# Kernel optimization log

Measured on AMD Instinct MI355X. Metric: run time of the kernel, lower is better.

The kernel has to match this reference:

```python
import jax, jax.numpy as jnp
import numpy as np

N_NODES = 50000
N_EDGES = 800000
IN_CH = 128
OUT_CH = 64
HEADS = 1
NEG_SLOPE = 0.2

def _glorot(key, shape):
    stdv = np.sqrt(6.0 / (shape[-2] + shape[-1]))
    return jax.random.uniform(key, shape, jnp.float32, -stdv, stdv)

def setup_inputs() -> dict:
    key = jax.random.key(0)
    k1, k2, k3, k4, k5 = jax.random.split(key, 5)
    x = jax.random.normal(k1, (N_NODES, IN_CH), jnp.float32)
    src = jax.random.randint(k2, (N_EDGES,), 0, N_NODES)
    dst = jax.random.randint(k3, (N_EDGES,), 0, N_NODES)
    # ensure no pre-existing self loops (remove_self_loops is then identity)
    dst = jnp.where(src == dst, (dst + 1) % N_NODES, dst)
    edge_index = jnp.stack([src, dst]).astype(jnp.int64)
    weight = _glorot(k4, (IN_CH, HEADS * OUT_CH))
    att = _glorot(k5, (1, HEADS, 2 * OUT_CH))
    bias = jnp.zeros((OUT_CH,), jnp.float32)
    return {"x": x, "edge_index": edge_index, "weight": weight, "att": att, "bias": bias}

def reference(x, edge_index, weight, att, bias):
    N = x.shape[0]
    # linear projection -> [N, heads, out]
    h = (x @ weight).reshape(N, HEADS, OUT_CH)
    # add self loops (input guaranteed free of self loops)
    loops = jnp.arange(N, dtype=edge_index.dtype)
    src = jnp.concatenate([edge_index[0], loops])  # source j
    dst = jnp.concatenate([edge_index[1], loops])  # target i
    x_j = h[src]   # [E+N, heads, out]
    x_i = h[dst]
    # attention logits: (cat([x_i, x_j]) * att).sum(-1) -> [E+N, heads]
    alpha = jnp.concatenate([x_i, x_j], axis=-1)
    alpha = (alpha * att).sum(axis=-1)
    alpha = jax.nn.leaky_relu(alpha, NEG_SLOPE)
    # segment softmax over destination nodes
    amax = jax.ops.segment_max(alpha, dst, num_segments=N)
    e = jnp.exp(alpha - amax[dst])
    esum = jax.ops.segment_sum(e, dst, num_segments=N)
    alpha = e / (esum[dst] + 1e-16)
    # message + scatter-add aggregation
    msg = x_j * alpha[:, :, None]
    out = jax.ops.segment_sum(msg, dst, num_segments=N)  # [N, heads, out]
    out = out.mean(axis=1) + bias
    # F.normalize (L2, dim=1, eps=1e-12); dropout is eval-mode identity
    norm = jnp.maximum(jnp.linalg.norm(out, axis=1, keepdims=True), 1e-12)
    return out / norm
```

## Files before the change

kernel.cpp:

```cpp
#include <hip/hip_runtime.h>
#include <math.h>

#define IN_CH 128
#define OUT_CH 64
#define NEG_SLOPE 0.2f
#define CAP 64

__device__ __forceinline__ unsigned short f2bf(float f) {
    unsigned u = __float_as_uint(f);
    unsigned r = (u + 0x7FFFu + ((u >> 16) & 1u)) >> 16;
    return (unsigned short)r;
}

__device__ __forceinline__ bool sniff_is64(const void* edges) {
    const unsigned* up = (const unsigned*)edges;
    bool is64 = true;
#pragma unroll
    for (int k = 0; k < 16; k++) is64 = is64 && (up[2 * k + 1] == 0u);
    return is64;
}

__global__ __launch_bounds__(256) void k_mm_cs(
        const float* __restrict__ x, const float* __restrict__ W,
        const float* __restrict__ att, unsigned short* __restrict__ h16,
        float* __restrict__ asrc, float* __restrict__ adst, int N,
        const void* __restrict__ edges, int* __restrict__ counts,
        int* __restrict__ slots, int* __restrict__ oflow_cnt,
        int2* __restrict__ oflow, int E, int mmb, int csb) {
    __shared__ float Ws[IN_CH * OUT_CH];
    int t = threadIdx.x;
    int bid = blockIdx.x;
    int lo = min(mmb, csb), M2 = 2 * lo;
    int role, id;
    if (bid < M2) { role = bid & 1; id = bid >> 1; }
    else          { role = (mmb > csb) ? 0 : 1; id = bid - M2 + lo; }

    if (role == 1) {
        int e0 = (id * 256 + t) * 4;
        if (e0 >= E) return;
        int s[4], d[4];
        bool full = (e0 + 3 < E);
        if (full) {
            if (sniff_is64(edges)) {
                const long long* p = (const long long*)edges;
#pragma unroll
                for (int i = 0; i < 4; i++) {
                    s[i] = (int)__builtin_nontemporal_load(p + e0 + i);
                    d[i] = (int)__builtin_nontemporal_load(p + (size_t)E + e0 + i);
                }
            } else {
                const int* p = (const int*)edges;
#pragma unroll
                for (int i = 0; i < 4; i++) {
                    s[i] = __builtin_nontemporal_load(p + e0 + i);
                    d[i] = __builtin_nontemporal_load(p + E + e0 + i);
                }
            }
#pragma unroll
            for (int i = 0; i < 4; i++) {
                int r = atomicAdd(counts + d[i], 1);
                if (r < CAP) {
                    slots[((size_t)d[i] << 6) + r] = s[i];
                } else {
                    int p2 = atomicAdd(oflow_cnt, 1);
                    oflow[p2] = make_int2(s[i], d[i]);
                }
            }
        } else {
            bool is64 = sniff_is64(edges);
            for (int i = 0; i < 4; i++) {
                if (e0 + i >= E) break;
                int sv, dv;
                if (is64) {
                    const long long* p = (const long long*)edges;
                    sv = (int)p[e0 + i];
                    dv = (int)p[(size_t)E + e0 + i];
                } else {
                    const int* p = (const int*)edges;
                    sv = p[e0 + i];
                    dv = p[E + e0 + i];
                }
                int r = atomicAdd(counts + dv, 1);
                if (r < CAP) {
                    slots[((size_t)dv << 6) + r] = sv;
                } else {
                    int p2 = atomicAdd(oflow_cnt, 1);
                    oflow[p2] = make_int2(sv, dv);
                }
            }
        }
        return;
    }

    for (int i = t * 4; i < IN_CH * OUT_CH; i += 256 * 4)
        *(float4*)&Ws[i] = *(const float4*)&W[i];
    int cg = t & 15, g = t >> 4;
    float4 att_d = *(const float4*)&att[cg * 4];
    float4 att_s = *(const float4*)&att[64 + cg * 4];
    __syncthreads();

    int n0 = id * 64 + g * 4;
    int nn[4];
#pragma unroll
    for (int m = 0; m < 4; m++) nn[m] = min(n0 + m, N - 1);

    float4 acc[4];
#pragma unroll
    for (int m = 0; m < 4; m++) acc[m] = make_float4(0.f, 0.f, 0.f, 0.f);

#pragma unroll 2
    for (int k4 = 0; k4 < IN_CH / 4; k4++) {
        float4 xv[4];
#pragma unroll
        for (int m = 0; m < 4; m++)
            xv[m] = *(const float4*)&x[(size_t)nn[m] * IN_CH + k4 * 4];
        float4 wv[4];
#pragma unroll
        for (int j = 0; j < 4; j++)
            wv[j] = *(const float4*)&Ws[(k4 * 4 + j) * OUT_CH + cg * 4];
#pragma unroll
        for (int m = 0; m < 4; m++) {
            acc[m].x = fmaf(xv[m].x, wv[0].x, acc[m].x);
            acc[m].y = fmaf(xv[m].x, wv[0].y, acc[m].y);
            acc[m].z = fmaf(xv[m].x, wv[0].z, acc[m].z);
            acc[m].w = fmaf(xv[m].x, wv[0].w, acc[m].w);
            acc[m].x = fmaf(xv[m].y, wv[1].x, acc[m].x);
            acc[m].y = fmaf(xv[m].y, wv[1].y, acc[m].y);
            acc[m].z = fmaf(xv[m].y, wv[1].z, acc[m].z);
            acc[m].w = fmaf(xv[m].y, wv[1].w, acc[m].w);
            acc[m].x = fmaf(xv[m].z, wv[2].x, acc[m].x);
            acc[m].y = fmaf(xv[m].z, wv[2].y, acc[m].y);
            acc[m].z = fmaf(xv[m].z, wv[2].z, acc[m].z);
            acc[m].w = fmaf(xv[m].z, wv[2].w, acc[m].w);
            acc[m].x = fmaf(xv[m].w, wv[3].x, acc[m].x);
            acc[m].y = fmaf(xv[m].w, wv[3].y, acc[m].y);
            acc[m].z = fmaf(xv[m].w, wv[3].z, acc[m].z);
            acc[m].w = fmaf(xv[m].w, wv[3].w, acc[m].w);
        }
    }

#pragma unroll
    for (int m = 0; m < 4; m++) {
        int node = n0 + m;
        if (node < N) {
            ushort4 hv;
            hv.x = f2bf(acc[m].x);
            hv.y = f2bf(acc[m].y);
            hv.z = f2bf(acc[m].z);
            hv.w = f2bf(acc[m].w);
            *(ushort4*)&h16[(size_t)node * OUT_CH + cg * 4] = hv;
        }
        float pd = acc[m].x * att_d.x + acc[m].y * att_d.y +
                   acc[m].z * att_d.z + acc[m].w * att_d.w;
        float ps = acc[m].x * att_s.x + acc[m].y * att_s.y +
                   acc[m].z * att_s.z + acc[m].w * att_s.w;
#pragma unroll
        for (int msk = 1; msk < 16; msk <<= 1) {
            pd += __shfl_xor(pd, msk, 64);
            ps += __shfl_xor(ps, msk, 64);
        }
        if (cg == 0 && node < N) { adst[node] = pd; asrc[node] = ps; }
    }
}

__global__ __launch_bounds__(256) void k_agg(const unsigned short* __restrict__ h16,
                                             const int* __restrict__ slots,
                                             const int* __restrict__ counts,
                                             const int* __restrict__ oflow_cnt,
                                             const int2* __restrict__ oflow,
                                             const float* __restrict__ asrc,
                                             const float* __restrict__ adst,
                                             const float* __restrict__ bias,
                                             float* __restrict__ out, int N) {
    __shared__ float2 stage[4][64];
    int lane = threadIdx.x & 63;
    int wid = threadIdx.x >> 6;
    int node = blockIdx.x * 4 + wid;
    if (node >= N) return;
    int half = lane >> 5;
    int ch2 = (lane & 31) * 2;

    float aD = adst[node];
    float a = aD + asrc[node];
    a = a > 0.f ? a : NEG_SLOPE * a;
    float w_self = __expf(a);
    unsigned hv = *(const unsigned*)&h16[(size_t)node * OUT_CH + ch2];
    float wse = half ? 0.f : w_self;
    float accx = wse * __uint_as_float(hv << 16);
    float accy = wse * __uint_as_float(hv & 0xFFFF0000u);

    int c = counts[node];
    int cs = min(c, CAP);
    int sv = 0;
    float wv = 0.f;
    if (lane < cs) {
        sv = slots[((size_t)node << 6) + lane];
        float av = aD + asrc[sv];
        av = av > 0.f ? av : NEG_SLOPE * av;
        wv = __expf(av);
    }
    float esum_lane = wv;
    stage[wid][lane] = make_float2(__int_as_float(sv), wv);

    for (int j = 0; j < cs; j += 16) {
#pragma unroll
        for (int k = 0; k < 8; k++) {
            float2 p = stage[wid][j + 2 * k + half];
            int s = __float_as_int(p.x);
            unsigned v = *(const unsigned*)&h16[((size_t)s << 6) + ch2];
            accx = fmaf(p.y, __uint_as_float(v << 16), accx);
            accy = fmaf(p.y, __uint_as_float(v & 0xFFFF0000u), accy);
        }
    }
    accx += __shfl_xor(accx, 32, 64);
    accy += __shfl_xor(accy, 32, 64);
#pragma unroll
    for (int m = 32; m >= 1; m >>= 1) esum_lane += __shfl_xor(esum_lane, m, 64);
    float esum = esum_lane + w_self;

    int oc = *oflow_cnt;
    if (oc > 0) {
        for (int i = 0; i < oc; i++) {
            int2 e = oflow[i];
            if (e.y == node) {
                float av = aD + asrc[e.x];
                av = av > 0.f ? av : NEG_SLOPE * av;
                float w = __expf(av);
                esum += w;
                unsigned v = *(const unsigned*)&h16[((size_t)e.x << 6) + ch2];
                accx = fmaf(w, __uint_as_float(v << 16), accx);
                accy = fmaf(w, __uint_as_float(v & 0xFFFF0000u), accy);
            }
        }
    }

    float inv = 1.f / (esum + 1e-16f);
    float2 bv = *(const float2*)&bias[ch2];
    float vx = accx * inv + bv.x;
    float vy = accy * inv + bv.y;
    float ss = vx * vx + vy * vy;
#pragma unroll
    for (int m = 16; m >= 1; m >>= 1) ss += __shfl_xor(ss, m, 64);
    float rinv = 1.f / fmaxf(sqrtf(ss), 1e-12f);
    if (!half)
        *(float2*)&out[(size_t)node * OUT_CH + ch2] = make_float2(vx * rinv, vy * rinv);
}

extern "C" void kernel_launch(void* const* d_in, const int* in_sizes, int n_in,
                              void* d_out, int out_size, void* d_ws, size_t ws_size,
                              hipStream_t stream) {
    const float* x    = (const float*)d_in[0];
    const void*  edges = d_in[1];
    const float* W    = (const float*)d_in[2];
    const float* att  = (const float*)d_in[3];
    const float* bias = (const float*)d_in[4];
    float* out = (float*)d_out;

    const int N = in_sizes[0] / IN_CH;
    const int E = in_sizes[1] / 2;
    const int MMB = (N + 63) / 64;
    const int CSB = (E + 1023) / 1024;

    char* ws = (char*)d_ws;
    size_t off = 0;
    auto alloc = [&](size_t bytes) -> void* {
        void* p = ws + off;
        off += bytes;
        off = (off + 255) & ~(size_t)255;
        return p;
    };
    int*            counts   = (int*)alloc((size_t)(N + 64) * 4);
    int*            slots    = (int*)alloc((size_t)N * CAP * 4);
    int2*           oflow    = (int2*)alloc((size_t)E * 8);
    unsigned short* h16      = (unsigned short*)alloc((size_t)N * OUT_CH * 2);
    float*          asrc     = (float*)alloc((size_t)N * 4);
    float*          adst     = (float*)alloc((size_t)N * 4);
    int*            oflow_cnt = counts + N;

    hipMemsetAsync(counts, 0, (size_t)(N + 64) * 4, stream);
    k_mm_cs<<<MMB + CSB, 256, 0, stream>>>(x, W, att, h16, asrc, adst, N,
                                           edges, counts, slots, oflow_cnt,
                                           oflow, E, MMB, CSB);
    k_agg<<<(N + 3) / 4, 256, 0, stream>>>(h16, slots, counts, oflow_cnt, oflow,
                                           asrc, adst, bias, out, N);
}
```

Measured before the change: 144.5 us.

## Fuse edge bucketing and projection per block, overlapping atomics with matmul

```diff
diff --git a/kernel.cpp b/kernel.cpp
--- a/kernel.cpp
+++ b/kernel.cpp
@@ -5,6 +5,10 @@
 #define OUT_CH 64
 #define NEG_SLOPE 0.2f
 #define CAP 64
+#define EPT 4
+
+typedef long long ll2 __attribute__((ext_vector_type(2)));
+typedef int i4v __attribute__((ext_vector_type(4)));
 
 __device__ __forceinline__ unsigned short f2bf(float f) {
     unsigned u = __float_as_uint(f);
@@ -26,140 +30,134 @@
         float* __restrict__ asrc, float* __restrict__ adst, int N,
         const void* __restrict__ edges, int* __restrict__ counts,
         int* __restrict__ slots, int* __restrict__ oflow_cnt,
-        int2* __restrict__ oflow, int E, int mmb, int csb) {
-    __shared__ float Ws[IN_CH * OUT_CH];
+        int2* __restrict__ oflow, int E) {
     int t = threadIdx.x;
     int bid = blockIdx.x;
-    int lo = min(mmb, csb), M2 = 2 * lo;
-    int role, id;
-    if (bid < M2) { role = bid & 1; id = bid >> 1; }
-    else          { role = (mmb > csb) ? 0 : 1; id = bid - M2 + lo; }
-
-    if (role == 1) {
-        int e0 = (id * 256 + t) * 4;
-        if (e0 >= E) return;
-        int s[4], d[4];
-        bool full = (e0 + 3 < E);
-        if (full) {
-            if (sniff_is64(edges)) {
+
+    int e0 = (bid * 256 + t) * EPT;
+    int s[EPT], d[EPT], r[EPT];
+    bool fullcs = (e0 + EPT <= E);
+    if (fullcs) {
+        if (sniff_is64(edges)) {
+            const ll2* ps = (const ll2*)((const long long*)edges + e0);
+            const ll2* pd = (const ll2*)((const long long*)edges + (size_t)E + e0);
+            ll2 v0 = __builtin_nontemporal_load(ps);
+            ll2 v1 = __builtin_nontemporal_load(ps + 1);
+            ll2 w0 = __builtin_nontemporal_load(pd);
+            ll2 w1 = __builtin_nontemporal_load(pd + 1);
+            s[0] = (int)v0.x; s[1] = (int)v0.y; s[2] = (int)v1.x; s[3] = (int)v1.y;
+            d[0] = (int)w0.x; d[1] = (int)w0.y; d[2] = (int)w1.x; d[3] = (int)w1.y;
+        } else {
+            i4v v = __builtin_nontemporal_load((const i4v*)((const int*)edges + e0));
+            i4v w = __builtin_nontemporal_load((const i4v*)((const int*)edges + E + e0));
+            s[0] = v.x; s[1] = v.y; s[2] = v.z; s[3] = v.w;
+            d[0] = w.x; d[1] = w.y; d[2] = w.z; d[3] = w.w;
+        }
+#pragma unroll
+        for (int i = 0; i < EPT; i++) r[i] = atomicAdd(counts + d[i], 1);
+    } else if (e0 < E) {
+        bool is64 = sniff_is64(edges);
+        for (int i = 0; i < EPT && e0 + i < E; i++) {
+            int sv, dv;
+            if (is64) {
                 const long long* p = (const long long*)edges;
-#pragma unroll
-                for (int i = 0; i < 4; i++) {
-                    s[i] = (int)__builtin_nontemporal_load(p + e0 + i);
-                    d[i] = (int)__builtin_nontemporal_load(p + (size_t)E + e0 + i);
-                }
+                sv = (int)p[e0 + i];
+                dv = (int)p[(size_t)E + e0 + i];
             } else {
                 const int* p = (const int*)edges;
-#pragma unroll
-                for (int i = 0; i < 4; i++) {
-                    s[i] = __builtin_nontemporal_load(p + e0 + i);
-                    d[i] = __builtin_nontemporal_load(p + E + e0 + i);
-                }
-            }
-#pragma unroll
-            for (int i = 0; i < 4; i++) {
-                int r = atomicAdd(counts + d[i], 1);
-                if (r < CAP) {
-                    slots[((size_t)d[i] << 6) + r] = s[i];
-                } else {
-                    int p2 = atomicAdd(oflow_cnt, 1);
-                    oflow[p2] = make_int2(s[i], d[i]);
-                }
-            }
-        } else {
-            bool is64 = sniff_is64(edges);
-            for (int i = 0; i < 4; i++) {
-                if (e0 + i >= E) break;
-                int sv, dv;
-                if (is64) {
-                    const long long* p = (const long long*)edges;
-                    sv = (int)p[e0 + i];
-                    dv = (int)p[(size_t)E + e0 + i];
-                } else {
-                    const int* p = (const int*)edges;
-                    sv = p[e0 + i];
-                    dv = p[E + e0 + i];
-                }
-                int r = atomicAdd(counts + dv, 1);
-                if (r < CAP) {
-                    slots[((size_t)dv << 6) + r] = sv;
-                } else {
-                    int p2 = atomicAdd(oflow_cnt, 1);
-                    oflow[p2] = make_int2(sv, dv);
-                }
-            }
-        }
-        return;
-    }
-
-    for (int i = t * 4; i < IN_CH * OUT_CH; i += 256 * 4)
-        *(float4*)&Ws[i] = *(const float4*)&W[i];
-    int cg = t & 15, g = t >> 4;
-    float4 att_d = *(const float4*)&att[cg * 4];
-    float4 att_s = *(const float4*)&att[64 + cg * 4];
-    __syncthreads();
-
-    int n0 = id * 64 + g * 4;
-    int nn[4];
-#pragma unroll
-    for (int m = 0; m < 4; m++) nn[m] = min(n0 + m, N - 1);
-
-    float4 acc[4];
-#pragma unroll
-    for (int m = 0; m < 4; m++) acc[m] = make_float4(0.f, 0.f, 0.f, 0.f);
+                sv = p[e0 + i];
+                dv = p[E + e0 + i];
+            }
+            int rr = atomicAdd(counts + dv, 1);
+            if (rr < CAP) {
+                slots[((size_t)dv << 6) + rr] = sv;
+            } else {
+                int p2 = atomicAdd(oflow_cnt, 1);
+                oflow[p2] = make_int2(sv, dv);
+            }
+        }
+    }
+    asm volatile("" ::: "memory");
+
+    if (bid * 64 < N) {
+        int cg = t & 15, g = t >> 4;
+        float4 att_d = *(const float4*)&att[cg * 4];
+        float4 att_s = *(const float4*)&att[64 + cg * 4];
+
+        int n0 = bid * 64 + g * 4;
+        int nn[4];
+#pragma unroll
+        for (int m = 0; m < 4; m++) nn[m] = min(n0 + m, N - 1);
+
+        float4 acc[4];
+#pragma unroll
+        for (int m = 0; m < 4; m++) acc[m] = make_float4(0.f, 0.f, 0.f, 0.f);
 
 #pragma unroll 2
-    for (int k4 = 0; k4 < IN_CH / 4; k4++) {
-        float4 xv[4];
-#pragma unroll
-        for (int m = 0; m < 4; m++)
-            xv[m] = *(const float4*)&x[(size_t)nn[m] * IN_CH + k4 * 4];
-        float4 wv[4];
-#pragma unroll
-        for (int j = 0; j < 4; j++)
-            wv[j] = *(const float4*)&Ws[(k4 * 4 + j) * OUT_CH + cg * 4];
+        for (int k4 = 0; k4 < IN_CH / 4; k4++) {
+            float4 xv[4];
+#pragma unroll
+            for (int m = 0; m < 4; m++)
+                xv[m] = *(const float4*)&x[(size_t)nn[m] * IN_CH + k4 * 4];
+            float4 wv[4];
+#pragma unroll
+            for (int j = 0; j < 4; j++)
+                wv[j] = *(const float4*)&W[(k4 * 4 + j) * OUT_CH + cg * 4];
+#pragma unroll
+            for (int m = 0; m < 4; m++) {
+                acc[m].x = fmaf(xv[m].x, wv[0].x, acc[m].x);
+                acc[m].y = fmaf(xv[m].x, wv[0].y, acc[m].y);
+                acc[m].z = fmaf(xv[m].x, wv[0].z, acc[m].z);
+                acc[m].w = fmaf(xv[m].x, wv[0].w, acc[m].w);
+                acc[m].x = fmaf(xv[m].y, wv[1].x, acc[m].x);
+                acc[m].y = fmaf(xv[m].y, wv[1].y, acc[m].y);
+                acc[m].z = fmaf(xv[m].y, wv[1].z, acc[m].z);
+                acc[m].w = fmaf(xv[m].y, wv[1].w, acc[m].w);
+                acc[m].x = fmaf(xv[m].z, wv[2].x, acc[m].x);
+                acc[m].y = fmaf(xv[m].z, wv[2].y, acc[m].y);
+                acc[m].z = fmaf(xv[m].z, wv[2].z, acc[m].z);
+                acc[m].w = fmaf(xv[m].z, wv[2].w, acc[m].w);
+                acc[m].x = fmaf(xv[m].w, wv[3].x, acc[m].x);
+                acc[m].y = fmaf(xv[m].w, wv[3].y, acc[m].y);
+                acc[m].z = fmaf(xv[m].w, wv[3].z, acc[m].z);
+                acc[m].w = fmaf(xv[m].w, wv[3].w, acc[m].w);
+            }
+        }
+
 #pragma unroll
         for (int m = 0; m < 4; m++) {
-            acc[m].x = fmaf(xv[m].x, wv[0].x, acc[m].x);
-            acc[m].y = fmaf(xv[m].x, wv[0].y, acc[m].y);
-            acc[m].z = fmaf(xv[m].x, wv[0].z, acc[m].z);
-            acc[m].w = fmaf(xv[m].x, wv[0].w, acc[m].w);
-            acc[m].x = fmaf(xv[m].y, wv[1].x, acc[m].x);
-            acc[m].y = fmaf(xv[m].y, wv[1].y, acc[m].y);
-            acc[m].z = fmaf(xv[m].y, wv[1].z, acc[m].z);
-            acc[m].w = fmaf(xv[m].y, wv[1].w, acc[m].w);
-            acc[m].x = fmaf(xv[m].z, wv[2].x, acc[m].x);
-            acc[m].y = fmaf(xv[m].z, wv[2].y, acc[m].y);
-            acc[m].z = fmaf(xv[m].z, wv[2].z, acc[m].z);
-            acc[m].w = fmaf(xv[m].z, wv[2].w, acc[m].w);
-            acc[m].x = fmaf(xv[m].w, wv[3].x, acc[m].x);
-            acc[m].y = fmaf(xv[m].w, wv[3].y, acc[m].y);
-            acc[m].z = fmaf(xv[m].w, wv[3].z, acc[m].z);
-            acc[m].w = fmaf(xv[m].w, wv[3].w, acc[m].w);
-        }
-    }
-
-#pragma unroll
-    for (int m = 0; m < 4; m++) {
-        int node = n0 + m;
-        if (node < N) {
-            ushort4 hv;
-            hv.x = f2bf(acc[m].x);
-            hv.y = f2bf(acc[m].y);
-            hv.z = f2bf(acc[m].z);
-            hv.w = f2bf(acc[m].w);
-            *(ushort4*)&h16[(size_t)node * OUT_CH + cg * 4] = hv;
-        }
-        float pd = acc[m].x * att_d.x + acc[m].y * att_d.y +
-                   acc[m].z * att_d.z + acc[m].w * att_d.w;
-        float ps = acc[m].x * att_s.x + acc[m].y * att_s.y +
-                   acc[m].z * att_s.z + acc[m].w * att_s.w;
-#pragma unroll
-        for (int msk = 1; msk < 16; msk <<= 1) {
-            pd += __shfl_xor(pd, msk, 64);
-            ps += __shfl_xor(ps, msk, 64);
-        }
-        if (cg == 0 && node < N) { adst[node] = pd; asrc[node] = ps; }
+            int node = n0 + m;
+            if (node < N) {
+                ushort4 hv;
+                hv.x = f2bf(acc[m].x);
+                hv.y = f2bf(acc[m].y);
+                hv.z = f2bf(acc[m].z);
+                hv.w = f2bf(acc[m].w);
+                *(ushort4*)&h16[(size_t)node * OUT_CH + cg * 4] = hv;
+            }
+            float pd = acc[m].x * att_d.x + acc[m].y * att_d.y +
+                       acc[m].z * att_d.z + acc[m].w * att_d.w;
+            float ps = acc[m].x * att_s.x + acc[m].y * att_s.y +
+                       acc[m].z * att_s.z + acc[m].w * att_s.w;
+#pragma unroll
+            for (int msk = 1; msk < 16; msk <<= 1) {
+                pd += __shfl_xor(pd, msk, 64);
+                ps += __shfl_xor(ps, msk, 64);
+            }
+            if (cg == 0 && node < N) { adst[node] = pd; asrc[node] = ps; }
+        }
+    }
+
+    if (fullcs) {
+#pragma unroll
+        for (int i = 0; i < EPT; i++) {
+            if (r[i] < CAP) {
+                slots[((size_t)d[i] << 6) + r[i]] = s[i];
+            } else {
+                int p2 = atomicAdd(oflow_cnt, 1);
+                oflow[p2] = make_int2(s[i], d[i]);
+            }
+        }
     }
 }
 
@@ -259,7 +257,8 @@
     const int N = in_sizes[0] / IN_CH;
     const int E = in_sizes[1] / 2;
     const int MMB = (N + 63) / 64;
-    const int CSB = (E + 1023) / 1024;
+    const int CSB = (E + 256 * EPT - 1) / (256 * EPT);
+    const int NB = MMB > CSB ? MMB : CSB;
 
     char* ws = (char*)d_ws;
     size_t off = 0;
@@ -278,9 +277,8 @@
     int*            oflow_cnt = counts + N;
 
     hipMemsetAsync(counts, 0, (size_t)(N + 64) * 4, stream);
-    k_mm_cs<<<MMB + CSB, 256, 0, stream>>>(x, W, att, h16, asrc, adst, N,
-                                           edges, counts, slots, oflow_cnt,
-                                           oflow, E, MMB, CSB);
+    k_mm_cs<<<NB, 256, 0, stream>>>(x, W, att, h16, asrc, adst, N,
+                                    edges, counts, slots, oflow_cnt, oflow, E);
     k_agg<<<(N + 3) / 4, 256, 0, stream>>>(h16, slots, counts, oflow_cnt, oflow,
                                            asrc, adst, bias, out, N);
 }
```

Result: slower. 172.6 us (+19.4%).

## Drop shared W staging, read weights from global, halve edges per thread

Applied to the files above, without the earlier changes.

```diff
diff --git a/kernel.cpp b/kernel.cpp
--- a/kernel.cpp
+++ b/kernel.cpp
@@ -5,6 +5,10 @@
 #define OUT_CH 64
 #define NEG_SLOPE 0.2f
 #define CAP 64
+#define EPT 2
+
+typedef long long ll2 __attribute__((ext_vector_type(2)));
+typedef int i2v __attribute__((ext_vector_type(2)));
 
 __device__ __forceinline__ unsigned short f2bf(float f) {
     unsigned u = __float_as_uint(f);
@@ -27,7 +31,6 @@
         const void* __restrict__ edges, int* __restrict__ counts,
         int* __restrict__ slots, int* __restrict__ oflow_cnt,
         int2* __restrict__ oflow, int E, int mmb, int csb) {
-    __shared__ float Ws[IN_CH * OUT_CH];
     int t = threadIdx.x;
     int bid = blockIdx.x;
     int lo = min(mmb, csb), M2 = 2 * lo;
@@ -36,68 +39,65 @@
     else          { role = (mmb > csb) ? 0 : 1; id = bid - M2 + lo; }
 
     if (role == 1) {
-        int e0 = (id * 256 + t) * 4;
+        int e0 = (id * 256 + t) * EPT;
         if (e0 >= E) return;
-        int s[4], d[4];
-        bool full = (e0 + 3 < E);
+        bool full = (e0 + 1 < E);
+        int s[2], d[2];
         if (full) {
             if (sniff_is64(edges)) {
+                ll2 v = __builtin_nontemporal_load(
+                    (const ll2*)((const long long*)edges + e0));
+                ll2 w = __builtin_nontemporal_load(
+                    (const ll2*)((const long long*)edges + (size_t)E + e0));
+                s[0] = (int)v.x; s[1] = (int)v.y;
+                d[0] = (int)w.x; d[1] = (int)w.y;
+            } else {
+                i2v v = __builtin_nontemporal_load(
+                    (const i2v*)((const int*)edges + e0));
+                i2v w = __builtin_nontemporal_load(
+                    (const i2v*)((const int*)edges + E + e0));
+                s[0] = v.x; s[1] = v.y;
+                d[0] = w.x; d[1] = w.y;
+            }
+            int r0 = atomicAdd(counts + d[0], 1);
+            int r1 = atomicAdd(counts + d[1], 1);
+            if (r0 < CAP) {
+                slots[((size_t)d[0] << 6) + r0] = s[0];
+            } else {
+                int p2 = atomicAdd(oflow_cnt, 1);
+                oflow[p2] = make_int2(s[0], d[0]);
+            }
+            if (r1 < CAP) {
+                slots[((size_t)d[1] << 6) + r1] = s[1];
+            } else {
+                int p2 = atomicAdd(oflow_cnt, 1);
+                oflow[p2] = make_int2(s[1], d[1]);
+            }
+        } else {
+            int sv, dv;
+            if (sniff_is64(edges)) {
                 const long long* p = (const long long*)edges;
-#pragma unroll
-                for (int i = 0; i < 4; i++) {
-                    s[i] = (int)__builtin_nontemporal_load(p + e0 + i);
-                    d[i] = (int)__builtin_nontemporal_load(p + (size_t)E + e0 + i);
-                }
+                sv = (int)p[e0];
+                dv = (int)p[(size_t)E + e0];
             } else {
                 const int* p = (const int*)edges;
-#pragma unroll
-                for (int i = 0; i < 4; i++) {
-                    s[i] = __builtin_nontemporal_load(p + e0 + i);
-                    d[i] = __builtin_nontemporal_load(p + E + e0 + i);
-                }
-            }
-#pragma unroll
-            for (int i = 0; i < 4; i++) {
-                int r = atomicAdd(counts + d[i], 1);
-                if (r < CAP) {
-                    slots[((size_t)d[i] << 6) + r] = s[i];
-                } else {
-                    int p2 = atomicAdd(oflow_cnt, 1);
-                    oflow[p2] = make_int2(s[i], d[i]);
-                }
-            }
-        } else {
-            bool is64 = sniff_is64(edges);
-            for (int i = 0; i < 4; i++) {
-                if (e0 + i >= E) break;
-                int sv, dv;
-                if (is64) {
-                    const long long* p = (const long long*)edges;
-                    sv = (int)p[e0 + i];
-                    dv = (int)p[(size_t)E + e0 + i];
-                } else {
-                    const int* p = (const int*)edges;
-                    sv = p[e0 + i];
-                    dv = p[E + e0 + i];
-                }
-                int r = atomicAdd(counts + dv, 1);
-                if (r < CAP) {
-                    slots[((size_t)dv << 6) + r] = sv;
-                } else {
-                    int p2 = atomicAdd(oflow_cnt, 1);
-                    oflow[p2] = make_int2(sv, dv);
-                }
+                sv = p[e0];
+                dv = p[E + e0];
+            }
+            int rr = atomicAdd(counts + dv, 1);
+            if (rr < CAP) {
+                slots[((size_t)dv << 6) + rr] = sv;
+            } else {
+                int p2 = atomicAdd(oflow_cnt, 1);
+                oflow[p2] = make_int2(sv, dv);
             }
         }
         return;
     }
 
-    for (int i = t * 4; i < IN_CH * OUT_CH; i += 256 * 4)
-        *(float4*)&Ws[i] = *(const float4*)&W[i];
     int cg = t & 15, g = t >> 4;
     float4 att_d = *(const float4*)&att[cg * 4];
     float4 att_s = *(const float4*)&att[64 + cg * 4];
-    __syncthreads();
 
     int n0 = id * 64 + g * 4;
     int nn[4];
@@ -117,7 +117,7 @@
         float4 wv[4];
 #pragma unroll
         for (int j = 0; j < 4; j++)
-            wv[j] = *(const float4*)&Ws[(k4 * 4 + j) * OUT_CH + cg * 4];
+            wv[j] = *(const float4*)&W[(k4 * 4 + j) * OUT_CH + cg * 4];
 #pragma unroll
         for (int m = 0; m < 4; m++) {
             acc[m].x = fmaf(xv[m].x, wv[0].x, acc[m].x);
@@ -259,7 +259,7 @@
     const int N = in_sizes[0] / IN_CH;
     const int E = in_sizes[1] / 2;
     const int MMB = (N + 63) / 64;
-    const int CSB = (E + 1023) / 1024;
+    const int CSB = (E + 256 * EPT - 1) / (256 * EPT);
 
     char* ws = (char*)d_ws;
     size_t off = 0;
```

Result: slower. 162.3 us (+12.4%).

## Shard edge scatter by destination range and rebalance fused matmul/scatter grid

Applied to the files above, without the earlier changes.

```diff
diff --git a/kernel.cpp b/kernel.cpp
--- a/kernel.cpp
+++ b/kernel.cpp
@@ -5,6 +5,13 @@
 #define OUT_CH 64
 #define NEG_SLOPE 0.2f
 #define CAP 64
+#define NSHARD 8
+#define SCAN_EPT 16
+
+typedef long long ll2 __attribute__((ext_vector_type(2)));
+typedef int i4v __attribute__((ext_vector_type(4)));
+typedef float f4v __attribute__((ext_vector_type(4)));
+typedef unsigned short us4v __attribute__((ext_vector_type(4)));
 
 __device__ __forceinline__ unsigned short f2bf(float f) {
     unsigned u = __float_as_uint(f);
@@ -26,66 +33,77 @@
         float* __restrict__ asrc, float* __restrict__ adst, int N,
         const void* __restrict__ edges, int* __restrict__ counts,
         int* __restrict__ slots, int* __restrict__ oflow_cnt,
-        int2* __restrict__ oflow, int E, int mmb, int csb) {
+        int2* __restrict__ oflow, int E, int groups) {
     __shared__ float Ws[IN_CH * OUT_CH];
     int t = threadIdx.x;
     int bid = blockIdx.x;
-    int lo = min(mmb, csb), M2 = 2 * lo;
-    int role, id;
-    if (bid < M2) { role = bid & 1; id = bid >> 1; }
-    else          { role = (mmb > csb) ? 0 : 1; id = bid - M2 + lo; }
+    int role, id = 0, shard = 0, chunk = 0;
+    if (bid >= groups * 24) {
+        role = 0; id = 8 * groups + (bid - groups * 24);
+    } else {
+        int g = bid / 24, p = bid % 24;
+        if (p < 16) { role = 1; shard = p & 7; chunk = g * 2 + (p >> 3); }
+        else        { role = 0; id = g * 8 + (p - 16); }
+    }
 
     if (role == 1) {
-        int e0 = (id * 256 + t) * 4;
-        if (e0 >= E) return;
-        int s[4], d[4];
-        bool full = (e0 + 3 < E);
-        if (full) {
-            if (sniff_is64(edges)) {
-                const long long* p = (const long long*)edges;
-#pragma unroll
-                for (int i = 0; i < 4; i++) {
-                    s[i] = (int)__builtin_nontemporal_load(p + e0 + i);
-                    d[i] = (int)__builtin_nontemporal_load(p + (size_t)E + e0 + i);
+        int lo = (int)(((long long)shard * N) / NSHARD);
+        int hi = (int)(((long long)(shard + 1) * N) / NSHARD);
+        int base = chunk * (256 * SCAN_EPT) + t * SCAN_EPT;
+        if (base >= E) return;
+        bool is64 = sniff_is64(edges);
+        int dv[SCAN_EPT];
+        if (base + SCAN_EPT <= E) {
+            if (is64) {
+                const ll2* pd = (const ll2*)((const long long*)edges + (size_t)E + base);
+#pragma unroll
+                for (int i = 0; i < SCAN_EPT / 2; i++) {
+                    ll2 w = __builtin_nontemporal_load(pd + i);
+                    dv[2 * i] = (int)w.x; dv[2 * i + 1] = (int)w.y;
                 }
             } else {
-                const int* p = (const int*)edges;
-#pragma unroll
-                for (int i = 0; i < 4; i++) {
-                    s[i] = __builtin_nontemporal_load(p + e0 + i);
-                    d[i] = __builtin_nontemporal_load(p + E + e0 + i);
+                const i4v* pd = (const i4v*)((const int*)edges + E + base);
+#pragma unroll
+                for (int i = 0; i < SCAN_EPT / 4; i++) {
+                    i4v w = __builtin_nontemporal_load(pd + i);
+                    dv[4 * i] = w.x; dv[4 * i + 1] = w.y;
+                    dv[4 * i + 2] = w.z; dv[4 * i + 3] = w.w;
                 }
             }
-#pragma unroll
-            for (int i = 0; i < 4; i++) {
-                int r = atomicAdd(counts + d[i], 1);
-                if (r < CAP) {
-                    slots[((size_t)d[i] << 6) + r] = s[i];
+        } else {
+            for (int i = 0; i < SCAN_EPT; i++) {
+                int e = base + i;
+                dv[i] = (e < E) ? (is64 ? (int)((const long long*)edges)[(size_t)E + e]
+                                        : ((const int*)edges)[E + e])
+                                : -1;
+            }
+        }
+        int sv[SCAN_EPT];
+        unsigned mmask = 0;
+#pragma unroll
+        for (int i = 0; i < SCAN_EPT; i++) {
+            int d = dv[i];
+            bool m = (d >= lo) && (d < hi);
+            if (m) {
+                sv[i] = is64 ? (int)__builtin_nontemporal_load(
+                                   (const long long*)edges + base + i)
+                             : __builtin_nontemporal_load(
+                                   (const int*)edges + base + i);
+                mmask |= (1u << i);
+            }
+        }
+        int rr[SCAN_EPT];
+#pragma unroll
+        for (int i = 0; i < SCAN_EPT; i++)
+            if (mmask & (1u << i)) rr[i] = atomicAdd(counts + dv[i], 1);
+#pragma unroll
+        for (int i = 0; i < SCAN_EPT; i++) {
+            if (mmask & (1u << i)) {
+                if (rr[i] < CAP) {
+                    slots[((size_t)dv[i] << 6) + rr[i]] = sv[i];
                 } else {
                     int p2 = atomicAdd(oflow_cnt, 1);
-                    oflow[p2] = make_int2(s[i], d[i]);
-                }
-            }
-        } else {
-            bool is64 = sniff_is64(edges);
-            for (int i = 0; i < 4; i++) {
-                if (e0 + i >= E) break;
-                int sv, dv;
-                if (is64) {
-                    const long long* p = (const long long*)edges;
-                    sv = (int)p[e0 + i];
-                    dv = (int)p[(size_t)E + e0 + i];
-                } else {
-                    const int* p = (const int*)edges;
-                    sv = p[e0 + i];
-                    dv = p[E + e0 + i];
-                }
-                int r = atomicAdd(counts + dv, 1);
-                if (r < CAP) {
-                    slots[((size_t)dv << 6) + r] = sv;
-                } else {
-                    int p2 = atomicAdd(oflow_cnt, 1);
-                    oflow[p2] = make_int2(sv, dv);
+                    oflow[p2] = make_int2(sv[i], dv[i]);
                 }
             }
         }
@@ -100,6 +118,7 @@
     __syncthreads();
 
     int n0 = id * 64 + g * 4;
+    if (n0 >= N + 3 && id * 64 >= N) {  }
     int nn[4];
 #pragma unroll
     for (int m = 0; m < 4; m++) nn[m] = min(n0 + m, N - 1);
@@ -110,10 +129,11 @@
 
 #pragma unroll 2
     for (int k4 = 0; k4 < IN_CH / 4; k4++) {
-        float4 xv[4];
+        f4v xv[4];
 #pragma unroll
         for (int m = 0; m < 4; m++)
-            xv[m] = *(const float4*)&x[(size_t)nn[m] * IN_CH + k4 * 4];
+            xv[m] = __builtin_nontemporal_load(
+                (const f4v*)&x[(size_t)nn[m] * IN_CH + k4 * 4]);
         float4 wv[4];
 #pragma unroll
         for (int j = 0; j < 4; j++)
@@ -143,12 +163,13 @@
     for (int m = 0; m < 4; m++) {
         int node = n0 + m;
         if (node < N) {
-            ushort4 hv;
+            us4v hv;
             hv.x = f2bf(acc[m].x);
             hv.y = f2bf(acc[m].y);
             hv.z = f2bf(acc[m].z);
             hv.w = f2bf(acc[m].w);
-            *(ushort4*)&h16[(size_t)node * OUT_CH + cg * 4] = hv;
+            __builtin_nontemporal_store(
+                hv, (us4v*)&h16[(size_t)node * OUT_CH + cg * 4]);
         }
         float pd = acc[m].x * att_d.x + acc[m].y * att_d.y +
                    acc[m].z * att_d.z + acc[m].w * att_d.w;
@@ -258,8 +279,14 @@
 
     const int N = in_sizes[0] / IN_CH;
     const int E = in_sizes[1] / 2;
+    const int CHUNK_E = 256 * SCAN_EPT;
+    int CHUNKS = (E + CHUNK_E - 1) / CHUNK_E;
+    CHUNKS = (CHUNKS + 1) & ~1;
+    const int GROUPS = CHUNKS / 2;
     const int MMB = (N + 63) / 64;
-    const int CSB = (E + 1023) / 1024;
+    int extra = MMB - 8 * GROUPS;
+    if (extra < 0) extra = 0;
+    const int grid = GROUPS * 24 + extra;
 
     char* ws = (char*)d_ws;
     size_t off = 0;
@@ -278,9 +305,9 @@
     int*            oflow_cnt = counts + N;
 
     hipMemsetAsync(counts, 0, (size_t)(N + 64) * 4, stream);
-    k_mm_cs<<<MMB + CSB, 256, 0, stream>>>(x, W, att, h16, asrc, adst, N,
-                                           edges, counts, slots, oflow_cnt,
-                                           oflow, E, MMB, CSB);
+    k_mm_cs<<<grid, 256, 0, stream>>>(x, W, att, h16, asrc, adst, N,
+                                      edges, counts, slots, oflow_cnt,
+                                      oflow, E, GROUPS);
     k_agg<<<(N + 3) / 4, 256, 0, stream>>>(h16, slots, counts, oflow_cnt, oflow,
                                            asrc, adst, bias, out, N);
 }
```

New measurement: 172.3 us. +19.2%, slower.
